# Kernel optimization log

Hardware: AMD Instinct MI355X
Metric: run time of the kernel (lower is better)

The kernel has to match this reference:

```python
import jax, jax.numpy as jnp
import numpy as np

N_NODES = 100000
N_EDGES = 1600000
HIDDEN = 64
OUT_CH = 16
N_GRAPHS = 64
IN_CH = 1


def setup_inputs() -> dict:
    key = jax.random.key(0)
    ks = jax.random.split(key, 16)
    x = jax.random.normal(ks[0], (N_NODES, IN_CH), dtype=jnp.float32)
    edge_index = jax.random.randint(ks[1], (2, N_EDGES), 0, N_NODES, dtype=jnp.int64)
    edge_weight = jax.random.uniform(ks[2], (N_EDGES,), dtype=jnp.float32)
    batch = jnp.sort(jax.random.randint(ks[3], (N_NODES,), 0, N_GRAPHS, dtype=jnp.int64))

    def glorot(k, shape):
        fan_in = shape[1]
        return jax.random.normal(k, shape, dtype=jnp.float32) / jnp.sqrt(jnp.float32(fan_in))

    return {
        "x": x, "edge_index": edge_index, "edge_weight": edge_weight, "batch": batch,
        "W_rel1": glorot(ks[4], (HIDDEN, IN_CH)), "b_rel1": jnp.zeros((HIDDEN,), jnp.float32),
        "W_root1": glorot(ks[5], (HIDDEN, IN_CH)),
        "W_rel2": glorot(ks[6], (HIDDEN, HIDDEN)), "b_rel2": jnp.zeros((HIDDEN,), jnp.float32),
        "W_root2": glorot(ks[7], (HIDDEN, HIDDEN)),
        "W_rel3": glorot(ks[8], (HIDDEN, HIDDEN)), "b_rel3": jnp.zeros((HIDDEN,), jnp.float32),
        "W_root3": glorot(ks[9], (HIDDEN, HIDDEN)),
        "W_lin": glorot(ks[10], (OUT_CH, HIDDEN)), "b_lin": jnp.zeros((OUT_CH,), jnp.float32),
    }


def graph_conv(x, src, dst, edge_weight, W_rel, b_rel, W_root):
    # PyG GraphConv (aggr='add'): lin_rel(sum_{j in N(i)} w_ij * x_j) + lin_root(x_i)
    msgs = x[src] * edge_weight[:, None]                      # [E, C]
    agg = jax.ops.segment_sum(msgs, dst, num_segments=N_NODES)  # [N, C]
    return agg @ W_rel.T + b_rel + x @ W_root.T


def reference(x, edge_index, edge_weight, batch,
              W_rel1, b_rel1, W_root1,
              W_rel2, b_rel2, W_root2,
              W_rel3, b_rel3, W_root3,
              W_lin, b_lin):
    src, dst = edge_index[0], edge_index[1]
    h = jax.nn.relu(graph_conv(x, src, dst, edge_weight, W_rel1, b_rel1, W_root1))
    h = jax.nn.relu(graph_conv(h, src, dst, edge_weight, W_rel2, b_rel2, W_root2))
    h = graph_conv(h, src, dst, edge_weight, W_rel3, b_rel3, W_root3)
    # global mean pool over graphs
    sums = jax.ops.segment_sum(h, batch, num_segments=N_GRAPHS)          # [G, H]
    counts = jax.ops.segment_sum(jnp.ones((h.shape[0],), h.dtype), batch,
                                 num_segments=N_GRAPHS)
    pooled = sums / jnp.maximum(counts, 1.0)[:, None]
    # dropout is identity in eval mode
    return pooled @ W_lin.T + b_lin                                       # [G, OUT_CH]
```

## Files before the change

### kernel.cpp

```cpp
#include <hip/hip_runtime.h>

#define N_NODES 100000
#define N_EDGES 1600000
#define HIDDEN 64
#define OUT_CH 16
#define N_GRAPHS 64
#define N_TILES 6250
#define SCAN_B 256
#define NB1 391
#define NBUCK 391
#define NN2 (NBUCK * 256)
#define CBLK 250
#define EPB 6400
#define W_SCALE (1.0f / 32767.0f)

typedef __attribute__((ext_vector_type(8))) short bf16x8;
typedef __attribute__((ext_vector_type(4))) float f32x4;

__device__ __forceinline__ float bfu(unsigned short u) {
    return __uint_as_float(((unsigned)u) << 16);
}
__device__ __forceinline__ unsigned short f2bf(float x) {
    unsigned u = __float_as_uint(x);
    return (unsigned short)((u + 0x7FFFu + ((u >> 16) & 1u)) >> 16);
}
__device__ __forceinline__ bf16x8 load_wfrag(const float* __restrict__ W, int c, int k0) {
    float4 a = *(const float4*)(W + c * 64 + k0);
    float4 b = *(const float4*)(W + c * 64 + k0 + 4);
    bf16x8 r;
    r[0] = (short)f2bf(a.x); r[1] = (short)f2bf(a.y); r[2] = (short)f2bf(a.z); r[3] = (short)f2bf(a.w);
    r[4] = (short)f2bf(b.x); r[5] = (short)f2bf(b.y); r[6] = (short)f2bf(b.z); r[7] = (short)f2bf(b.w);
    return r;
}

__global__ __launch_bounds__(256) void k_bhist(const int* __restrict__ dst, int* __restrict__ bmat) {
    __shared__ int bh[NBUCK];
    int t = threadIdx.x, blk = blockIdx.x;
    for (int b = t; b < NBUCK; b += 256) bh[b] = 0;
    __syncthreads();
    int base = blk * EPB;
    for (int r = 0; r < EPB / 256; ++r)
        atomicAdd(&bh[dst[base + r * 256 + t] >> 8], 1);
    __syncthreads();
    for (int b = t; b < NBUCK; b += 256) bmat[b * 256 + blk] = bh[b];
}

__global__ __launch_bounds__(256) void k_colscan(int* __restrict__ bmat, int* __restrict__ btotal) {
    __shared__ int s[256];
    int b = blockIdx.x, t = threadIdx.x;
    int v = (t < CBLK) ? bmat[b * 256 + t] : 0;
    s[t] = v;
    __syncthreads();
    for (int off = 1; off < 256; off <<= 1) {
        int x = (t >= off) ? s[t - off] : 0;
        __syncthreads();
        s[t] += x;
        __syncthreads();
    }
    if (t < CBLK) bmat[b * 256 + t] = s[t] - v;
    if (t == 255) btotal[b] = s[255];
}

__global__ __launch_bounds__(512) void k_scan_bsum(const int* __restrict__ in, int* __restrict__ outp) {
    __shared__ int s[512];
    int t = threadIdx.x;
    int v = (t < NB1) ? in[t] : 0;
    s[t] = v;
    __syncthreads();
    for (int off = 1; off < 512; off <<= 1) {
        int x = (t >= off) ? s[t - off] : 0;
        __syncthreads();
        s[t] += x;
        __syncthreads();
    }
    if (t < NB1) outp[t] = s[t] - v;
}

__global__ __launch_bounds__(256) void k_coarse(
    const int* __restrict__ src, const int* __restrict__ dst, const float* __restrict__ w,
    const int* __restrict__ bmat, const int* __restrict__ cbase, uint2* __restrict__ C)
{
    __shared__ int cur[NBUCK];
    int t = threadIdx.x, blk = blockIdx.x;
    for (int b = t; b < NBUCK; b += 256) cur[b] = cbase[b] + bmat[b * 256 + blk];
    __syncthreads();
    int base = blk * EPB;
    for (int r = 0; r < EPB / 256; ++r) {
        int e = base + r * 256 + t;
        int d = dst[e];
        int q = __float2int_rn(w[e] * 32767.0f);
        unsigned pe = ((unsigned)src[e] << 15) | (unsigned)q;
        int pos = atomicAdd(&cur[d >> 8], 1);
        C[pos] = make_uint2(pe, (unsigned)(d & 255));
    }
}

__global__ __launch_bounds__(256) void k_fhist(const uint2* __restrict__ C, const int* __restrict__ cbase,
                                               const int* __restrict__ btotal, int* __restrict__ pcnt) {
    __shared__ int c[256];
    int b = blockIdx.x, t = threadIdx.x;
    c[t] = 0;
    __syncthreads();
    int j0 = cbase[b], j1 = j0 + btotal[b];
    for (int j = j0 + t; j < j1; j += 256) atomicAdd(&c[C[j].y], 1);
    __syncthreads();
    pcnt[b * 256 + t] = c[t];
}

__global__ __launch_bounds__(SCAN_B) void k_partial(const int* __restrict__ pcnt, int* __restrict__ bsum) {
    __shared__ int s[SCAN_B];
    int b = blockIdx.x, t = threadIdx.x;
    s[t] = (pcnt[b * SCAN_B + t] + 3) & ~3;
    __syncthreads();
    for (int off = SCAN_B / 2; off > 0; off >>= 1) {
        if (t < off) s[t] += s[t + off];
        __syncthreads();
    }
    if (t == 0) bsum[b] = s[0];
}

__global__ __launch_bounds__(SCAN_B) void k_scan_final(const int* __restrict__ pcnt, const int* __restrict__ boff,
                                                       int* __restrict__ row_ptr) {
    __shared__ int s[SCAN_B];
    int b = blockIdx.x, t = threadIdx.x;
    int i = b * SCAN_B + t;
    int v = (pcnt[i] + 3) & ~3;
    s[t] = v;
    __syncthreads();
    for (int off = 1; off < SCAN_B; off <<= 1) {
        int x = (t >= off) ? s[t - off] : 0;
        __syncthreads();
        s[t] += x;
        __syncthreads();
    }
    row_ptr[i] = boff[b] + s[t] - v;
    if (i == NN2 - 1) row_ptr[NN2] = boff[b] + s[t];
}

__global__ __launch_bounds__(256) void k_fine(const uint2* __restrict__ C, const int* __restrict__ cbase,
                                              const int* __restrict__ btotal, const int* __restrict__ row_ptr,
                                              unsigned* __restrict__ E) {
    __shared__ int cur[256];
    int b = blockIdx.x, t = threadIdx.x;
    cur[t] = row_ptr[b * 256 + t];
    __syncthreads();
    int j0 = cbase[b], j1 = j0 + btotal[b];
    for (int j = j0 + t; j < j1; j += 256) {
        uint2 c = C[j];
        int pos = atomicAdd(&cur[c.y], 1);
        E[pos] = c.x;
    }
}

__global__ __launch_bounds__(256) void k_agg1_pair(const int* __restrict__ rp, const unsigned* __restrict__ E,
                                                   const float* __restrict__ x, float2* __restrict__ p) {
    int i = blockIdx.x * 256 + threadIdx.x;
    if (i >= N_NODES) return;
    int j1 = rp[i + 1];
    float acc = 0.0f;
    for (int j = rp[i]; j < j1; ++j) {
        unsigned e = E[j];
        acc = fmaf((float)(e & 32767u) * W_SCALE, x[e >> 15], acc);
    }
    p[i] = make_float2(acc, x[i]);
}

__global__ __launch_bounds__(256) void k_gather_pair(
    const int* __restrict__ rp, const unsigned* __restrict__ E,
    const float2* __restrict__ p,
    const float* __restrict__ Wr1, const float* __restrict__ b1,
    const float* __restrict__ Wo1, unsigned short* __restrict__ agg)
{
    int t = blockIdx.x * 256 + threadIdx.x;
    int node = t >> 6, c = t & 63;
    if (node >= N_NODES) return;
    float wr = Wr1[c], bb = b1[c], wo = Wo1[c];
    int j0 = rp[node], j1 = rp[node + 1];
    const uint4* E4 = (const uint4*)E;
    float acc = 0.0f;
    for (int j4 = (j0 >> 2); j4 < (j1 >> 2); ++j4) {
        uint4 e = E4[j4];
        float2 p0 = p[e.x >> 15];
        float2 p1 = p[e.y >> 15];
        float2 p2 = p[e.z >> 15];
        float2 p3 = p[e.w >> 15];
        float w0 = (float)(e.x & 32767u) * W_SCALE;
        float w1 = (float)(e.y & 32767u) * W_SCALE;
        float w2 = (float)(e.z & 32767u) * W_SCALE;
        float w3 = (float)(e.w & 32767u) * W_SCALE;
        acc = fmaf(w0, fmaxf(fmaf(p0.x, wr, fmaf(p0.y, wo, bb)), 0.0f), acc);
        acc = fmaf(w1, fmaxf(fmaf(p1.x, wr, fmaf(p1.y, wo, bb)), 0.0f), acc);
        acc = fmaf(w2, fmaxf(fmaf(p2.x, wr, fmaf(p2.y, wo, bb)), 0.0f), acc);
        acc = fmaf(w3, fmaxf(fmaf(p3.x, wr, fmaf(p3.y, wo, bb)), 0.0f), acc);
    }
    agg[node * 64 + c] = f2bf(acc);
}

__global__ __launch_bounds__(256) void k_gather_bf16(
    const int* __restrict__ rp, const unsigned* __restrict__ E,
    const unsigned short* __restrict__ h2, unsigned short* __restrict__ agg)
{
    int t = blockIdx.x * 256 + threadIdx.x;
    int node = t >> 6;
    int l = t & 63;
    int g = l >> 4, q = l & 15;
    if (node >= N_NODES) return;
    int j0 = rp[node], j1 = rp[node + 1];
    float4 acc = make_float4(0.0f, 0.0f, 0.0f, 0.0f);
    int j = j0;
    unsigned ec = (j < j1) ? E[j + g] : 0u;
    while (j < j1) {
        int jn = j + 4;
        unsigned src = ec >> 15;
        float wq = (float)(ec & 32767u) * W_SCALE;
        ushort4 rv = *((const ushort4*)(h2 + src * 64) + q);
        unsigned en = (jn < j1) ? E[jn + g] : 0u;
        acc.x = fmaf(wq, bfu(rv.x), acc.x);
        acc.y = fmaf(wq, bfu(rv.y), acc.y);
        acc.z = fmaf(wq, bfu(rv.z), acc.z);
        acc.w = fmaf(wq, bfu(rv.w), acc.w);
        ec = en; j = jn;
    }
    acc.x += __shfl_xor(acc.x, 16); acc.y += __shfl_xor(acc.y, 16);
    acc.z += __shfl_xor(acc.z, 16); acc.w += __shfl_xor(acc.w, 16);
    acc.x += __shfl_xor(acc.x, 32); acc.y += __shfl_xor(acc.y, 32);
    acc.z += __shfl_xor(acc.z, 32); acc.w += __shfl_xor(acc.w, 32);
    if (l < 16) {
        ushort4 st;
        st.x = f2bf(acc.x); st.y = f2bf(acc.y); st.z = f2bf(acc.z); st.w = f2bf(acc.w);
        ((ushort4*)(agg + node * 64))[q] = st;
    }
}

__global__ __launch_bounds__(256) void k_transform2_mfma(
    const unsigned short* __restrict__ agg, const float2* __restrict__ p,
    const float* __restrict__ Wrel, const float* __restrict__ brel,
    const float* __restrict__ Wroot,
    const float* __restrict__ Wr1, const float* __restrict__ b1,
    const float* __restrict__ Wo1,
    unsigned short* __restrict__ h2)
{
    int t = threadIdx.x;
    int wv = t >> 6, l = t & 63;
    int lo = l & 15, hi = l >> 4;
    bf16x8 wR[4][2], wO[4][2];
    #pragma unroll
    for (int ct = 0; ct < 4; ++ct)
        #pragma unroll
        for (int kh = 0; kh < 2; ++kh) {
            wR[ct][kh] = load_wfrag(Wrel,  ct * 16 + lo, kh * 32 + hi * 8);
            wO[ct][kh] = load_wfrag(Wroot, ct * 16 + lo, kh * 32 + hi * 8);
        }
    float bias[4][4];
    #pragma unroll
    for (int ct = 0; ct < 4; ++ct)
        #pragma unroll
        for (int j = 0; j < 4; ++j) bias[ct][j] = brel[ct * 16 + hi * 4 + j];
    float w1a[16], w1b[16], w1c[16];
    #pragma unroll
    for (int kh = 0; kh < 2; ++kh)
        #pragma unroll
        for (int j = 0; j < 8; ++j) {
            int idx = kh * 32 + hi * 8 + j;
            w1a[kh * 8 + j] = Wr1[idx]; w1b[kh * 8 + j] = Wo1[idx]; w1c[kh * 8 + j] = b1[idx];
        }
    int wid = blockIdx.x * 4 + wv, nw = gridDim.x * 4;
    for (int tile = wid; tile < N_TILES; tile += nw) {
        int i = tile * 16 + lo;
        float2 pv = p[i];
        bf16x8 bA0 = *(const bf16x8*)(agg + i * 64 + hi * 8);
        bf16x8 bA1 = *(const bf16x8*)(agg + i * 64 + 32 + hi * 8);
        bf16x8 bH0, bH1;
        #pragma unroll
        for (int j = 0; j < 8; ++j) {
            float h0 = fmaxf(fmaf(pv.x, w1a[j],     fmaf(pv.y, w1b[j],     w1c[j])),     0.0f);
            float h1 = fmaxf(fmaf(pv.x, w1a[8 + j], fmaf(pv.y, w1b[8 + j], w1c[8 + j])), 0.0f);
            bH0[j] = (short)f2bf(h0);
            bH1[j] = (short)f2bf(h1);
        }
        #pragma unroll
        for (int ct = 0; ct < 4; ++ct) {
            f32x4 acc = {bias[ct][0], bias[ct][1], bias[ct][2], bias[ct][3]};
            acc = __builtin_amdgcn_mfma_f32_16x16x32_bf16(wR[ct][0], bA0, acc, 0, 0, 0);
            acc = __builtin_amdgcn_mfma_f32_16x16x32_bf16(wR[ct][1], bA1, acc, 0, 0, 0);
            acc = __builtin_amdgcn_mfma_f32_16x16x32_bf16(wO[ct][0], bH0, acc, 0, 0, 0);
            acc = __builtin_amdgcn_mfma_f32_16x16x32_bf16(wO[ct][1], bH1, acc, 0, 0, 0);
            ushort4 st;
            st.x = f2bf(fmaxf(acc[0], 0.0f)); st.y = f2bf(fmaxf(acc[1], 0.0f));
            st.z = f2bf(fmaxf(acc[2], 0.0f)); st.w = f2bf(fmaxf(acc[3], 0.0f));
            *(ushort4*)(h2 + i * 64 + ct * 16 + hi * 4) = st;
        }
    }
}

__device__ __forceinline__ void flush_pool(float* pool, int gcur, float* __restrict__ sums,
                                           int lo, int hi) {
    #pragma unroll
    for (int n = 0; n < 16; ++n) {
        float v = pool[n];
        v += __shfl_xor(v, 1); v += __shfl_xor(v, 2);
        v += __shfl_xor(v, 4); v += __shfl_xor(v, 8);
        if (lo == 0) atomicAdd(&sums[gcur * 64 + (n >> 2) * 16 + hi * 4 + (n & 3)], v);
        pool[n] = 0.0f;
    }
}

__global__ __launch_bounds__(256) void k_transform3_pool_mfma(
    const unsigned short* __restrict__ agg, const unsigned short* __restrict__ h2,
    const float* __restrict__ Wrel, const float* __restrict__ brel,
    const float* __restrict__ Wroot, const int* __restrict__ batch,
    float* __restrict__ sums)
{
    int t = threadIdx.x;
    int wv = t >> 6, l = t & 63;
    int lo = l & 15, hi = l >> 4;
    bf16x8 wR[4][2], wO[4][2];
    #pragma unroll
    for (int ct = 0; ct < 4; ++ct)
        #pragma unroll
        for (int kh = 0; kh < 2; ++kh) {
            wR[ct][kh] = load_wfrag(Wrel,  ct * 16 + lo, kh * 32 + hi * 8);
            wO[ct][kh] = load_wfrag(Wroot, ct * 16 + lo, kh * 32 + hi * 8);
        }
    float bias[4][4];
    #pragma unroll
    for (int ct = 0; ct < 4; ++ct)
        #pragma unroll
        for (int j = 0; j < 4; ++j) bias[ct][j] = brel[ct * 16 + hi * 4 + j];

    int nw = gridDim.x * 4;
    int wid = blockIdx.x * 4 + wv;
    int tpw = (N_TILES + nw - 1) / nw;
    int t0 = wid * tpw, t1 = min(t0 + tpw, N_TILES);
    if (t0 >= t1) return;

    float pool[16];
    #pragma unroll
    for (int n = 0; n < 16; ++n) pool[n] = 0.0f;
    int gcur = batch[t0 * 16];

    for (int tile = t0; tile < t1; ++tile) {
        int i = tile * 16 + lo;
        int gi = batch[i];
        bf16x8 bA0 = *(const bf16x8*)(agg + i * 64 + hi * 8);
        bf16x8 bA1 = *(const bf16x8*)(agg + i * 64 + 32 + hi * 8);
        bf16x8 bH0 = *(const bf16x8*)(h2  + i * 64 + hi * 8);
        bf16x8 bH1 = *(const bf16x8*)(h2  + i * 64 + 32 + hi * 8);
        f32x4 acc[4];
        #pragma unroll
        for (int ct = 0; ct < 4; ++ct) {
            f32x4 a = {bias[ct][0], bias[ct][1], bias[ct][2], bias[ct][3]};
            a = __builtin_amdgcn_mfma_f32_16x16x32_bf16(wR[ct][0], bA0, a, 0, 0, 0);
            a = __builtin_amdgcn_mfma_f32_16x16x32_bf16(wR[ct][1], bA1, a, 0, 0, 0);
            a = __builtin_amdgcn_mfma_f32_16x16x32_bf16(wO[ct][0], bH0, a, 0, 0, 0);
            a = __builtin_amdgcn_mfma_f32_16x16x32_bf16(wO[ct][1], bH1, a, 0, 0, 0);
            acc[ct] = a;
        }
        int gfirst = __shfl(gi, 0);
        int glast  = __shfl(gi, 15);
        if (gfirst != glast) {
            flush_pool(pool, gcur, sums, lo, hi);
            #pragma unroll
            for (int ct = 0; ct < 4; ++ct)
                #pragma unroll
                for (int j = 0; j < 4; ++j)
                    atomicAdd(&sums[gi * 64 + ct * 16 + hi * 4 + j], acc[ct][j]);
            gcur = glast;
        } else {
            if (gfirst != gcur) {
                flush_pool(pool, gcur, sums, lo, hi);
                gcur = gfirst;
            }
            #pragma unroll
            for (int ct = 0; ct < 4; ++ct)
                #pragma unroll
                for (int j = 0; j < 4; ++j) pool[ct * 4 + j] += acc[ct][j];
        }
    }
    flush_pool(pool, gcur, sums, lo, hi);
}

__global__ __launch_bounds__(64) void k_pool2(
    const float* __restrict__ sums, const int* __restrict__ batch,
    const float* __restrict__ Wlin, const float* __restrict__ blin,
    float* __restrict__ out)
{
    int g = blockIdx.x;
    int c = threadIdx.x;
    int lo = 0, hi = N_NODES;
    while (lo < hi) { int mid = (lo + hi) >> 1; if (batch[mid] < g) lo = mid + 1; else hi = mid; }
    int s0 = lo;
    lo = 0; hi = N_NODES;
    while (lo < hi) { int mid = (lo + hi) >> 1; if (batch[mid] < g + 1) lo = mid + 1; else hi = mid; }
    int s1 = lo;
    __shared__ float pooled[64];
    float cnt = (float)(s1 - s0);
    pooled[c] = sums[g * 64 + c] / fmaxf(cnt, 1.0f);
    __syncthreads();
    if (c < OUT_CH) {
        float acc = blin[c];
        #pragma unroll 8
        for (int k = 0; k < HIDDEN; ++k) acc += pooled[k] * Wlin[c * 64 + k];
        out[g * OUT_CH + c] = acc;
    }
}

extern "C" void kernel_launch(void* const* d_in, const int* in_sizes, int n_in,
                              void* d_out, int out_size, void* d_ws, size_t ws_size,
                              hipStream_t stream)
{
    const float* x    = (const float*)d_in[0];
    const int*   ei   = (const int*)d_in[1];
    const int*   src  = ei;
    const int*   dst  = ei + N_EDGES;
    const float* ew   = (const float*)d_in[2];
    const int*   batch= (const int*)d_in[3];
    const float* Wr1  = (const float*)d_in[4];
    const float* b1   = (const float*)d_in[5];
    const float* Wo1  = (const float*)d_in[6];
    const float* Wr2  = (const float*)d_in[7];
    const float* b2   = (const float*)d_in[8];
    const float* Wo2  = (const float*)d_in[9];
    const float* Wr3  = (const float*)d_in[10];
    const float* b3   = (const float*)d_in[11];
    const float* Wo3  = (const float*)d_in[12];
    const float* Wlin = (const float*)d_in[13];
    const float* blin = (const float*)d_in[14];
    float* out = (float*)d_out;

    char* ws = (char*)d_ws;
    const size_t K = 1024;
    int*            row_ptr = (int*)(ws + 0);
    int*            bmat    = (int*)(ws + 512 * K);
    int*            btotal  = (int*)(ws + 1024 * K);
    int*            cbase   = (int*)(ws + 1028 * K);
    int*            bsum    = (int*)(ws + 1032 * K);
    int*            boff    = (int*)(ws + 1036 * K);
    int*            pcnt    = (int*)(ws + 1040 * K);
    float*          sums    = (float*)(ws + 1444 * K);
    float2*         p       = (float2*)(ws + 1536 * K);
    uint2*          C       = (uint2*)(ws + 2560 * K);
    unsigned*       E       = (unsigned*)(ws + 15360 * K);
    unsigned short* h2      = (unsigned short*)(ws + 23552 * K);
    unsigned short* aggbuf  = (unsigned short*)(ws + 36864 * K);

    hipMemsetAsync(E, 0, 7800 * K, stream);
    hipMemsetAsync(sums, 0, N_GRAPHS * HIDDEN * sizeof(float), stream);
    k_bhist<<<CBLK, 256, 0, stream>>>(dst, bmat);
    k_colscan<<<NBUCK, 256, 0, stream>>>(bmat, btotal);
    k_scan_bsum<<<1, 512, 0, stream>>>(btotal, cbase);
    k_coarse<<<CBLK, 256, 0, stream>>>(src, dst, ew, bmat, cbase, C);
    k_fhist<<<NBUCK, 256, 0, stream>>>(C, cbase, btotal, pcnt);
    k_partial<<<NB1, SCAN_B, 0, stream>>>(pcnt, bsum);
    k_scan_bsum<<<1, 512, 0, stream>>>(bsum, boff);
    k_scan_final<<<NB1, SCAN_B, 0, stream>>>(pcnt, boff, row_ptr);
    k_fine<<<NBUCK, 256, 0, stream>>>(C, cbase, btotal, row_ptr, E);

    k_agg1_pair<<<NB1, 256, 0, stream>>>(row_ptr, E, x, p);

    k_gather_pair<<<(N_NODES * 64) / 256, 256, 0, stream>>>(row_ptr, E, p, Wr1, b1, Wo1, aggbuf);
    k_transform2_mfma<<<512, 256, 0, stream>>>(aggbuf, p, Wr2, b2, Wo2, Wr1, b1, Wo1, h2);

    k_gather_bf16<<<(N_NODES * 64) / 256, 256, 0, stream>>>(row_ptr, E, h2, aggbuf);
    k_transform3_pool_mfma<<<512, 256, 0, stream>>>(aggbuf, h2, Wr3, b3, Wo3, batch, sums);

    k_pool2<<<N_GRAPHS, 64, 0, stream>>>(sums, batch, Wlin, blin, out);
}
```

Baseline: 330.6 us.

## Fuse layer-1 scalar aggregation into fine scatter; restructure gathers with edge-parallel lanes

```diff
diff --git a/kernel.cpp b/kernel.cpp
--- a/kernel.cpp
+++ b/kernel.cpp
@@ -139,10 +139,12 @@
 
 __global__ __launch_bounds__(256) void k_fine(const uint2* __restrict__ C, const int* __restrict__ cbase,
                                               const int* __restrict__ btotal, const int* __restrict__ row_ptr,
-                                              unsigned* __restrict__ E) {
+                                              const float* __restrict__ x,
+                                              unsigned* __restrict__ E, float2* __restrict__ p) {
     __shared__ int cur[256];
     int b = blockIdx.x, t = threadIdx.x;
-    cur[t] = row_ptr[b * 256 + t];
+    int rp0 = row_ptr[b * 256 + t];
+    cur[t] = rp0;
     __syncthreads();
     int j0 = cbase[b], j1 = j0 + btotal[b];
     for (int j = j0 + t; j < j1; j += 256) {
@@ -150,19 +152,17 @@
         int pos = atomicAdd(&cur[c.y], 1);
         E[pos] = c.x;
     }
-}
-
-__global__ __launch_bounds__(256) void k_agg1_pair(const int* __restrict__ rp, const unsigned* __restrict__ E,
-                                                   const float* __restrict__ x, float2* __restrict__ p) {
-    int i = blockIdx.x * 256 + threadIdx.x;
-    if (i >= N_NODES) return;
-    int j1 = rp[i + 1];
-    float acc = 0.0f;
-    for (int j = rp[i]; j < j1; ++j) {
-        unsigned e = E[j];
-        acc = fmaf((float)(e & 32767u) * W_SCALE, x[e >> 15], acc);
-    }
-    p[i] = make_float2(acc, x[i]);
+    __syncthreads();
+    int i = b * 256 + t;
+    if (i < N_NODES) {
+        int jend = cur[t];
+        float acc = 0.0f;
+        for (int j = rp0; j < jend; ++j) {
+            unsigned e = E[j];
+            acc = fmaf((float)(e & 32767u) * W_SCALE, x[e >> 15], acc);
+        }
+        p[i] = make_float2(acc, x[i]);
+    }
 }
 
 __global__ __launch_bounds__(256) void k_gather_pair(
@@ -172,28 +172,47 @@
     const float* __restrict__ Wo1, unsigned short* __restrict__ agg)
 {
     int t = blockIdx.x * 256 + threadIdx.x;
-    int node = t >> 6, c = t & 63;
+    int node = t >> 6;
+    int l = t & 63;
+    int g = l >> 4, q = l & 15;
     if (node >= N_NODES) return;
-    float wr = Wr1[c], bb = b1[c], wo = Wo1[c];
+    float4 wr = *(const float4*)(Wr1 + q * 4);
+    float4 wo = *(const float4*)(Wo1 + q * 4);
+    float4 bb = *(const float4*)(b1  + q * 4);
     int j0 = rp[node], j1 = rp[node + 1];
-    const uint4* E4 = (const uint4*)E;
-    float acc = 0.0f;
-    for (int j4 = (j0 >> 2); j4 < (j1 >> 2); ++j4) {
-        uint4 e = E4[j4];
-        float2 p0 = p[e.x >> 15];
-        float2 p1 = p[e.y >> 15];
-        float2 p2 = p[e.z >> 15];
-        float2 p3 = p[e.w >> 15];
-        float w0 = (float)(e.x & 32767u) * W_SCALE;
-        float w1 = (float)(e.y & 32767u) * W_SCALE;
-        float w2 = (float)(e.z & 32767u) * W_SCALE;
-        float w3 = (float)(e.w & 32767u) * W_SCALE;
-        acc = fmaf(w0, fmaxf(fmaf(p0.x, wr, fmaf(p0.y, wo, bb)), 0.0f), acc);
-        acc = fmaf(w1, fmaxf(fmaf(p1.x, wr, fmaf(p1.y, wo, bb)), 0.0f), acc);
-        acc = fmaf(w2, fmaxf(fmaf(p2.x, wr, fmaf(p2.y, wo, bb)), 0.0f), acc);
-        acc = fmaf(w3, fmaxf(fmaf(p3.x, wr, fmaf(p3.y, wo, bb)), 0.0f), acc);
-    }
-    agg[node * 64 + c] = f2bf(acc);
+    float4 a0 = make_float4(0.f, 0.f, 0.f, 0.f);
+    float4 a1 = make_float4(0.f, 0.f, 0.f, 0.f);
+    int j = j0;
+    unsigned ec0 = (j     < j1) ? E[j + g]     : 0u;
+    unsigned ec1 = (j + 4 < j1) ? E[j + 4 + g] : 0u;
+    while (j < j1) {
+        float2 p0 = p[ec0 >> 15];
+        float2 p1 = p[ec1 >> 15];
+        unsigned en0 = (j + 8  < j1) ? E[j + 8 + g]  : 0u;
+        unsigned en1 = (j + 12 < j1) ? E[j + 12 + g] : 0u;
+        float w0 = (float)(ec0 & 32767u) * W_SCALE;
+        float w1 = (float)(ec1 & 32767u) * W_SCALE;
+        a0.x = fmaf(w0, fmaxf(fmaf(p0.x, wr.x, fmaf(p0.y, wo.x, bb.x)), 0.0f), a0.x);
+        a0.y = fmaf(w0, fmaxf(fmaf(p0.x, wr.y, fmaf(p0.y, wo.y, bb.y)), 0.0f), a0.y);
+        a0.z = fmaf(w0, fmaxf(fmaf(p0.x, wr.z, fmaf(p0.y, wo.z, bb.z)), 0.0f), a0.z);
+        a0.w = fmaf(w0, fmaxf(fmaf(p0.x, wr.w, fmaf(p0.y, wo.w, bb.w)), 0.0f), a0.w);
+        a1.x = fmaf(w1, fmaxf(fmaf(p1.x, wr.x, fmaf(p1.y, wo.x, bb.x)), 0.0f), a1.x);
+        a1.y = fmaf(w1, fmaxf(fmaf(p1.x, wr.y, fmaf(p1.y, wo.y, bb.y)), 0.0f), a1.y);
+        a1.z = fmaf(w1, fmaxf(fmaf(p1.x, wr.z, fmaf(p1.y, wo.z, bb.z)), 0.0f), a1.z);
+        a1.w = fmaf(w1, fmaxf(fmaf(p1.x, wr.w, fmaf(p1.y, wo.w, bb.w)), 0.0f), a1.w);
+        ec0 = en0; ec1 = en1; j += 8;
+    }
+    float4 acc;
+    acc.x = a0.x + a1.x; acc.y = a0.y + a1.y; acc.z = a0.z + a1.z; acc.w = a0.w + a1.w;
+    acc.x += __shfl_xor(acc.x, 16); acc.y += __shfl_xor(acc.y, 16);
+    acc.z += __shfl_xor(acc.z, 16); acc.w += __shfl_xor(acc.w, 16);
+    acc.x += __shfl_xor(acc.x, 32); acc.y += __shfl_xor(acc.y, 32);
+    acc.z += __shfl_xor(acc.z, 32); acc.w += __shfl_xor(acc.w, 32);
+    if (l < 16) {
+        ushort4 st;
+        st.x = f2bf(acc.x); st.y = f2bf(acc.y); st.z = f2bf(acc.z); st.w = f2bf(acc.w);
+        ((ushort4*)(agg + node * 64))[q] = st;
+    }
 }
 
 __global__ __launch_bounds__(256) void k_gather_bf16(
@@ -206,21 +225,30 @@
     int g = l >> 4, q = l & 15;
     if (node >= N_NODES) return;
     int j0 = rp[node], j1 = rp[node + 1];
-    float4 acc = make_float4(0.0f, 0.0f, 0.0f, 0.0f);
+    float4 a0 = make_float4(0.f, 0.f, 0.f, 0.f);
+    float4 a1 = make_float4(0.f, 0.f, 0.f, 0.f);
     int j = j0;
-    unsigned ec = (j < j1) ? E[j + g] : 0u;
+    unsigned ec0 = (j     < j1) ? E[j + g]     : 0u;
+    unsigned ec1 = (j + 4 < j1) ? E[j + 4 + g] : 0u;
     while (j < j1) {
-        int jn = j + 4;
-        unsigned src = ec >> 15;
-        float wq = (float)(ec & 32767u) * W_SCALE;
-        ushort4 rv = *((const ushort4*)(h2 + src * 64) + q);
-        unsigned en = (jn < j1) ? E[jn + g] : 0u;
-        acc.x = fmaf(wq, bfu(rv.x), acc.x);
-        acc.y = fmaf(wq, bfu(rv.y), acc.y);
-        acc.z = fmaf(wq, bfu(rv.z), acc.z);
-        acc.w = fmaf(wq, bfu(rv.w), acc.w);
-        ec = en; j = jn;
-    }
+        ushort4 r0 = *((const ushort4*)(h2 + (ec0 >> 15) * 64) + q);
+        ushort4 r1 = *((const ushort4*)(h2 + (ec1 >> 15) * 64) + q);
+        unsigned en0 = (j + 8  < j1) ? E[j + 8 + g]  : 0u;
+        unsigned en1 = (j + 12 < j1) ? E[j + 12 + g] : 0u;
+        float w0 = (float)(ec0 & 32767u) * W_SCALE;
+        float w1 = (float)(ec1 & 32767u) * W_SCALE;
+        a0.x = fmaf(w0, bfu(r0.x), a0.x);
+        a0.y = fmaf(w0, bfu(r0.y), a0.y);
+        a0.z = fmaf(w0, bfu(r0.z), a0.z);
+        a0.w = fmaf(w0, bfu(r0.w), a0.w);
+        a1.x = fmaf(w1, bfu(r1.x), a1.x);
+        a1.y = fmaf(w1, bfu(r1.y), a1.y);
+        a1.z = fmaf(w1, bfu(r1.z), a1.z);
+        a1.w = fmaf(w1, bfu(r1.w), a1.w);
+        ec0 = en0; ec1 = en1; j += 8;
+    }
+    float4 acc;
+    acc.x = a0.x + a1.x; acc.y = a0.y + a1.y; acc.z = a0.z + a1.z; acc.w = a0.w + a1.w;
     acc.x += __shfl_xor(acc.x, 16); acc.y += __shfl_xor(acc.y, 16);
     acc.z += __shfl_xor(acc.z, 16); acc.w += __shfl_xor(acc.w, 16);
     acc.x += __shfl_xor(acc.x, 32); acc.y += __shfl_xor(acc.y, 32);
@@ -454,9 +482,7 @@
     k_partial<<<NB1, SCAN_B, 0, stream>>>(pcnt, bsum);
     k_scan_bsum<<<1, 512, 0, stream>>>(bsum, boff);
     k_scan_final<<<NB1, SCAN_B, 0, stream>>>(pcnt, boff, row_ptr);
-    k_fine<<<NBUCK, 256, 0, stream>>>(C, cbase, btotal, row_ptr, E);
-
-    k_agg1_pair<<<NB1, 256, 0, stream>>>(row_ptr, E, x, p);
+    k_fine<<<NBUCK, 256, 0, stream>>>(C, cbase, btotal, row_ptr, x, E, p);
 
     k_gather_pair<<<(N_NODES * 64) / 256, 256, 0, stream>>>(row_ptr, E, p, Wr1, b1, Wo1, aggbuf);
     k_transform2_mfma<<<512, 256, 0, stream>>>(aggbuf, p, Wr2, b2, Wo2, Wr1, b1, Wo1, h2);
```

Result: faster. 295.7 us (-10.5%).
